# Optimization experiments

Hardware: AMD Instinct MI355X
Metric: run time of the kernel (lower is better)

Reference implementation:

```python
import jax, jax.numpy as jnp
import numpy as np

B, S, D = 4, 2048, 64
H = 16            # num_heads
HD = D // H       # head_dim = 4 (code's misnamed 'num_heads' variable)
EPS = 1e-5        # BatchNorm1d default eps


def setup_inputs() -> dict:
    key = jax.random.key(0)
    ks = jax.random.split(key, 8)
    sc = 1.0 / np.sqrt(D)
    return {
        "x": jax.random.normal(ks[0], (B, S, D), dtype=jnp.float32),
        "Wq": jax.random.normal(ks[1], (D, D), dtype=jnp.float32) * sc,
        "bq": jnp.zeros((D,), dtype=jnp.float32),
        "Wk": jax.random.normal(ks[2], (D, D), dtype=jnp.float32) * sc,
        "bk": jnp.zeros((D,), dtype=jnp.float32),
        "Wv": jax.random.normal(ks[3], (D, D), dtype=jnp.float32) * sc,
        "bv": jnp.zeros((D,), dtype=jnp.float32),
        "gamma": jnp.ones((D,), dtype=jnp.float32),
        "beta": jnp.zeros((D,), dtype=jnp.float32),
    }


def reference(x, Wq, bq, Wk, bk, Wv, bv, gamma, beta):
    # ReLU-activated QKV projections
    Q = jax.nn.relu(jnp.einsum("bsd,de->bse", x, Wq) + bq)
    K = jax.nn.relu(jnp.einsum("bsd,de->bse", x, Wk) + bk)
    V = jax.nn.relu(jnp.einsum("bsd,de->bse", x, Wv) + bv)

    # split(dim=2)->cat(dim=0) is equivalent to head-split reshape [B,S,H,HD]
    Qh = Q.reshape(B, S, H, HD)
    Kh = K.reshape(B, S, H, HD)
    Vh = V.reshape(B, S, H, HD)

    scores = jnp.einsum("bqhd,bkhd->bhqk", Qh, Kh) / jnp.sqrt(jnp.float32(HD))
    attn = jax.nn.softmax(scores, axis=-1)  # dropout_rate = 0.0 -> no-op
    out = jnp.einsum("bhqk,bkhd->bqhd", attn, Vh).reshape(B, S, D)

    # residual
    out = out + x

    # BatchNorm1d(64) in training mode: batch stats over (B, S) per channel
    mean = jnp.mean(out, axis=(0, 1))
    var = jnp.var(out, axis=(0, 1))  # biased variance, as used for normalization
    out = (out - mean) * jax.lax.rsqrt(var + EPS) * gamma + beta
    return out
```

## Files before the change

### kernel.cpp

```cpp
#include <hip/hip_runtime.h>

#define BB 4
#define SS 2048
#define DD 64
#define HH 16
#define HDD 4
#define NBH (BB*HH)
#define NROWS (BB*SS)
#define CHK 512
#define LOG2E_HALF 0.7213475204444817f

typedef float f32x2 __attribute__((ext_vector_type(2)));

__global__ __launch_bounds__(256) void qkv_kernel(
    const float* __restrict__ x,
    const float* __restrict__ Wq, const float* __restrict__ bq,
    const float* __restrict__ Wk, const float* __restrict__ bk,
    const float* __restrict__ Wv, const float* __restrict__ bv,
    float* __restrict__ Q, float* __restrict__ KV)
{
    __shared__ float xs[4 * 64];
    const int tid = threadIdx.x;
    const int row0 = blockIdx.x * 4;

    xs[tid] = x[(size_t)row0 * 64 + tid];
    __syncthreads();

    const int r = tid >> 6;
    const int c = tid & 63;
    const int row = row0 + r;
    const int b = row >> 11;
    const int s = row & (SS - 1);
    const float* xr = &xs[r * 64];

    float aq = bq[c], ak = bk[c], av = bv[c];
    #pragma unroll 16
    for (int k = 0; k < 64; ++k) {
        const float xv = xr[k];
        aq = fmaf(xv, Wq[k * 64 + c], aq);
        ak = fmaf(xv, Wk[k * 64 + c], ak);
        av = fmaf(xv, Wv[k * 64 + c], av);
    }
    aq = fmaxf(aq, 0.0f);
    ak = fmaxf(ak, 0.0f) * LOG2E_HALF;
    av = fmaxf(av, 0.0f);

    const int h = c >> 2, hd = c & 3;
    const size_t bhs = ((size_t)(b * HH + h) * SS + s);
    Q[bhs * 4 + hd] = aq;

    const int p = s >> 1, po = s & 1;
    const size_t pb = ((size_t)(b * HH + h) * (SS / 2) + p) * 16;
    KV[pb + hd * 2 + po] = ak;
    KV[pb + 8 + hd * 2 + po] = av;
}

__global__ __launch_bounds__(256) void attn_bn_kernel(
    const float* __restrict__ Qb, const float* __restrict__ KVb,
    const float* __restrict__ x, float* __restrict__ y,
    float* __restrict__ part2)
{
    __shared__ float4 kvs4[CHK * 4];
    __shared__ float rr[4][8];
    const f32x2* kvs = (const f32x2*)kvs4;

    const int tid = threadIdx.x;
    const int bh = blockIdx.x >> 3;
    const int qt = blockIdx.x & 7;
    const int qrow = qt * 256 + tid;

    const float4 q4 = ((const float4*)Qb)[(size_t)bh * SS + qrow];
    const f32x2 qx = {q4.x, q4.x}, qy = {q4.y, q4.y};
    const f32x2 qz = {q4.z, q4.z}, qw = {q4.w, q4.w};

    f32x2 acx = {0.f, 0.f}, acy = {0.f, 0.f};
    f32x2 acz = {0.f, 0.f}, acw = {0.f, 0.f};
    f32x2 sm = {0.f, 0.f};

    const float4* kvg = (const float4*)(KVb + (size_t)bh * (SS / 2) * 16);

    for (int ch = 0; ch < SS / 2 / CHK; ++ch) {
        __syncthreads();
        #pragma unroll
        for (int i = 0; i < CHK * 4 / 256; ++i)
            kvs4[i * 256 + tid] = kvg[ch * CHK * 4 + i * 256 + tid];
        __syncthreads();

        #pragma unroll 2
        for (int j = 0; j < CHK; ++j) {
            const f32x2 kx = kvs[j * 8 + 0];
            const f32x2 ky = kvs[j * 8 + 1];
            const f32x2 kz = kvs[j * 8 + 2];
            const f32x2 kw = kvs[j * 8 + 3];
            const f32x2 vx = kvs[j * 8 + 4];
            const f32x2 vy = kvs[j * 8 + 5];
            const f32x2 vz = kvs[j * 8 + 6];
            const f32x2 vw = kvs[j * 8 + 7];
            f32x2 s = qx * kx;
            s = __builtin_elementwise_fma(qy, ky, s);
            s = __builtin_elementwise_fma(qz, kz, s);
            s = __builtin_elementwise_fma(qw, kw, s);
            f32x2 e;
            e.x = __builtin_amdgcn_exp2f(s.x);
            e.y = __builtin_amdgcn_exp2f(s.y);
            sm += e;
            acx = __builtin_elementwise_fma(e, vx, acx);
            acy = __builtin_elementwise_fma(e, vy, acy);
            acz = __builtin_elementwise_fma(e, vz, acz);
            acw = __builtin_elementwise_fma(e, vw, acw);
        }
    }

    const float sum = sm.x + sm.y;
    const float inv = 1.0f / sum;
    const int b = bh >> 4, h = bh & 15;
    const size_t o = ((size_t)(b * SS + qrow)) * DD + h * HDD;
    const float4 xr = *(const float4*)(x + o);
    float4 out;
    out.x = fmaf(acx.x + acx.y, inv, xr.x);
    out.y = fmaf(acy.x + acy.y, inv, xr.y);
    out.z = fmaf(acz.x + acz.y, inv, xr.z);
    out.w = fmaf(acw.x + acw.y, inv, xr.w);
    *(float4*)(y + o) = out;

    float v[8] = {out.x, out.y, out.z, out.w,
                  out.x * out.x, out.y * out.y, out.z * out.z, out.w * out.w};
    #pragma unroll
    for (int i = 0; i < 8; ++i) {
        float t = v[i];
        for (int off = 32; off > 0; off >>= 1) t += __shfl_down(t, off);
        v[i] = t;
    }
    const int wid = tid >> 6;
    if ((tid & 63) == 0) {
        #pragma unroll
        for (int i = 0; i < 8; ++i) rr[wid][i] = v[i];
    }
    __syncthreads();
    if (tid < 8) {
        const float t = rr[0][tid] + rr[1][tid] + rr[2][tid] + rr[3][tid];
        const int slot = b * 8 + qt;
        const int i = tid & 3;
        const int c = h * 4 + i;
        if (tid < 4) part2[c * 32 + slot] = t;
        else         part2[2048 + c * 32 + slot] = t;
    }
}

__global__ __launch_bounds__(256) void bn_norm_fused(
    float* __restrict__ y, const float* __restrict__ part2,
    const float* __restrict__ gamma, const float* __restrict__ beta)
{
    __shared__ float st[128];
    const int tid = threadIdx.x;
    if (tid < 128) {
        const int c = tid & 63;
        const float* p = part2 + (tid >> 6) * 2048 + c * 32;
        float s = 0.f;
        #pragma unroll
        for (int i = 0; i < 32; ++i) s += p[i];
        st[tid] = s;
    }
    __syncthreads();

    const int idx = blockIdx.x * 256 + tid;
    const int c0 = (idx & 15) * 4;
    float4 v = ((const float4*)y)[idx];
    const float n = 1.0f / NROWS;
    const float m0 = st[c0] * n,     m1 = st[c0 + 1] * n;
    const float m2 = st[c0 + 2] * n, m3 = st[c0 + 3] * n;
    const float r0 = rsqrtf(st[64 + c0] * n - m0 * m0 + 1e-5f);
    const float r1 = rsqrtf(st[65 + c0] * n - m1 * m1 + 1e-5f);
    const float r2 = rsqrtf(st[66 + c0] * n - m2 * m2 + 1e-5f);
    const float r3 = rsqrtf(st[67 + c0] * n - m3 * m3 + 1e-5f);
    float4 o;
    o.x = fmaf((v.x - m0) * r0, gamma[c0],     beta[c0]);
    o.y = fmaf((v.y - m1) * r1, gamma[c0 + 1], beta[c0 + 1]);
    o.z = fmaf((v.z - m2) * r2, gamma[c0 + 2], beta[c0 + 2]);
    o.w = fmaf((v.w - m3) * r3, gamma[c0 + 3], beta[c0 + 3]);
    ((float4*)y)[idx] = o;
}

extern "C" void kernel_launch(void* const* d_in, const int* in_sizes, int n_in,
                              void* d_out, int out_size, void* d_ws, size_t ws_size,
                              hipStream_t stream)
{
    const float* x     = (const float*)d_in[0];
    const float* Wq    = (const float*)d_in[1];
    const float* bq    = (const float*)d_in[2];
    const float* Wk    = (const float*)d_in[3];
    const float* bk    = (const float*)d_in[4];
    const float* Wv    = (const float*)d_in[5];
    const float* bv    = (const float*)d_in[6];
    const float* gamma = (const float*)d_in[7];
    const float* beta  = (const float*)d_in[8];
    float* out = (float*)d_out;

    float* ws    = (float*)d_ws;
    float* Q     = ws;
    float* KV    = ws + 524288;
    float* part2 = ws + 1572864;

    qkv_kernel<<<NROWS / 4, 256, 0, stream>>>(x, Wq, bq, Wk, bk, Wv, bv, Q, KV);
    attn_bn_kernel<<<NBH * 8, 256, 0, stream>>>(Q, KV, x, out, part2);
    bn_norm_fused<<<NROWS * DD / 1024, 256, 0, stream>>>(out, part2, gamma, beta);
}
```

Before: 119.3 us.

## Split attention over key chunks with atomic-counter last-block reduction

Each attention block now handles two query rows per thread (QR=2), so every K/V value loaded from shared memory is reused across two queries. The key dimension is split into KSPLIT slices across separate blocks. Partial accumulators and sums go to workspace, and the last-arriving block, detected with an atomic counter, combines them and computes the residual and BatchNorm partial sums. The aim is more blocks for better occupancy and more reuse of LDS loads. The cost is extra global traffic for the partials, fence and atomic synchronisation, and a split factor that depends on the workspace size.

```diff
diff --git a/kernel.cpp b/kernel.cpp
--- a/kernel.cpp
+++ b/kernel.cpp
@@ -7,18 +7,25 @@
 #define HDD 4
 #define NBH (BB*HH)
 #define NROWS (BB*SS)
-#define CHK 512
+#define NQ (NBH*SS)
 #define LOG2E_HALF 0.7213475204444817f
 
 typedef float f32x2 __attribute__((ext_vector_type(2)));
+
+#define QR 2
+#define QTN (SS/(256*QR))
+#define NGRP (NBH*QTN)
 
 __global__ __launch_bounds__(256) void qkv_kernel(
     const float* __restrict__ x,
     const float* __restrict__ Wq, const float* __restrict__ bq,
     const float* __restrict__ Wk, const float* __restrict__ bk,
     const float* __restrict__ Wv, const float* __restrict__ bv,
-    float* __restrict__ Q, float* __restrict__ KV)
-{
+    float* __restrict__ Q, float* __restrict__ KV,
+    unsigned int* __restrict__ cnt)
+{
+    if (blockIdx.x == 0) cnt[threadIdx.x] = 0u;
+
     __shared__ float xs[4 * 64];
     const int tid = threadIdx.x;
     const int row0 = blockIdx.x * 4;
@@ -55,95 +62,142 @@
     KV[pb + 8 + hd * 2 + po] = av;
 }
 
-__global__ __launch_bounds__(256) void attn_bn_kernel(
+template<int KSPLIT>
+__global__ __launch_bounds__(256) void attn_kernel(
     const float* __restrict__ Qb, const float* __restrict__ KVb,
     const float* __restrict__ x, float* __restrict__ y,
-    float* __restrict__ part2)
-{
-    __shared__ float4 kvs4[CHK * 4];
+    float* __restrict__ accS, float* __restrict__ sumS,
+    float* __restrict__ part2, unsigned int* __restrict__ cnt)
+{
+    constexpr int PAIRS = SS / 2 / KSPLIT;
+    __shared__ float4 kvs4[PAIRS * 4];
     __shared__ float rr[4][8];
+    __shared__ unsigned int oldv;
     const f32x2* kvs = (const f32x2*)kvs4;
 
     const int tid = threadIdx.x;
-    const int bh = blockIdx.x >> 3;
-    const int qt = blockIdx.x & 7;
-    const int qrow = qt * 256 + tid;
-
-    const float4 q4 = ((const float4*)Qb)[(size_t)bh * SS + qrow];
-    const f32x2 qx = {q4.x, q4.x}, qy = {q4.y, q4.y};
-    const f32x2 qz = {q4.z, q4.z}, qw = {q4.w, q4.w};
-
-    f32x2 acx = {0.f, 0.f}, acy = {0.f, 0.f};
-    f32x2 acz = {0.f, 0.f}, acw = {0.f, 0.f};
-    f32x2 sm = {0.f, 0.f};
-
-    const float4* kvg = (const float4*)(KVb + (size_t)bh * (SS / 2) * 16);
-
-    for (int ch = 0; ch < SS / 2 / CHK; ++ch) {
-        __syncthreads();
-        #pragma unroll
-        for (int i = 0; i < CHK * 4 / 256; ++i)
-            kvs4[i * 256 + tid] = kvg[ch * CHK * 4 + i * 256 + tid];
-        __syncthreads();
-
-        #pragma unroll 2
-        for (int j = 0; j < CHK; ++j) {
-            const f32x2 kx = kvs[j * 8 + 0];
-            const f32x2 ky = kvs[j * 8 + 1];
-            const f32x2 kz = kvs[j * 8 + 2];
-            const f32x2 kw = kvs[j * 8 + 3];
-            const f32x2 vx = kvs[j * 8 + 4];
-            const f32x2 vy = kvs[j * 8 + 5];
-            const f32x2 vz = kvs[j * 8 + 6];
-            const f32x2 vw = kvs[j * 8 + 7];
-            f32x2 s = qx * kx;
-            s = __builtin_elementwise_fma(qy, ky, s);
-            s = __builtin_elementwise_fma(qz, kz, s);
-            s = __builtin_elementwise_fma(qw, kw, s);
+    int blk = blockIdx.x;
+    const int ks = blk / (NBH * QTN);
+    blk -= ks * (NBH * QTN);
+    const int bh = blk / QTN;
+    const int qt = blk - bh * QTN;
+
+    const float4* kvg = (const float4*)(KVb + ((size_t)bh * (SS / 2) + (size_t)ks * PAIRS) * 16);
+    #pragma unroll
+    for (int i = 0; i < PAIRS * 4 / 256; ++i)
+        kvs4[i * 256 + tid] = kvg[i * 256 + tid];
+
+    f32x2 qx[QR], qy[QR], qz[QR], qw[QR];
+    #pragma unroll
+    for (int r = 0; r < QR; ++r) {
+        const int qrow = qt * (256 * QR) + r * 256 + tid;
+        const float4 q = ((const float4*)Qb)[(size_t)bh * SS + qrow];
+        qx[r] = {q.x, q.x}; qy[r] = {q.y, q.y};
+        qz[r] = {q.z, q.z}; qw[r] = {q.w, q.w};
+    }
+
+    f32x2 acx[QR], acy[QR], acz[QR], acw[QR], sm[QR];
+    #pragma unroll
+    for (int r = 0; r < QR; ++r) {
+        acx[r] = {0.f, 0.f}; acy[r] = {0.f, 0.f};
+        acz[r] = {0.f, 0.f}; acw[r] = {0.f, 0.f};
+        sm[r] = {0.f, 0.f};
+    }
+
+    __syncthreads();
+
+    #pragma unroll 2
+    for (int j = 0; j < PAIRS; ++j) {
+        const f32x2 kx = kvs[j * 8 + 0];
+        const f32x2 ky = kvs[j * 8 + 1];
+        const f32x2 kz = kvs[j * 8 + 2];
+        const f32x2 kw = kvs[j * 8 + 3];
+        const f32x2 vx = kvs[j * 8 + 4];
+        const f32x2 vy = kvs[j * 8 + 5];
+        const f32x2 vz = kvs[j * 8 + 6];
+        const f32x2 vw = kvs[j * 8 + 7];
+        #pragma unroll
+        for (int r = 0; r < QR; ++r) {
+            f32x2 s = qx[r] * kx;
+            s = __builtin_elementwise_fma(qy[r], ky, s);
+            s = __builtin_elementwise_fma(qz[r], kz, s);
+            s = __builtin_elementwise_fma(qw[r], kw, s);
             f32x2 e;
             e.x = __builtin_amdgcn_exp2f(s.x);
             e.y = __builtin_amdgcn_exp2f(s.y);
-            sm += e;
-            acx = __builtin_elementwise_fma(e, vx, acx);
-            acy = __builtin_elementwise_fma(e, vy, acy);
-            acz = __builtin_elementwise_fma(e, vz, acz);
-            acw = __builtin_elementwise_fma(e, vw, acw);
+            sm[r] += e;
+            acx[r] = __builtin_elementwise_fma(e, vx, acx[r]);
+            acy[r] = __builtin_elementwise_fma(e, vy, acy[r]);
+            acz[r] = __builtin_elementwise_fma(e, vz, acz[r]);
+            acw[r] = __builtin_elementwise_fma(e, vw, acw[r]);
         }
     }
 
-    const float sum = sm.x + sm.y;
-    const float inv = 1.0f / sum;
+    #pragma unroll
+    for (int r = 0; r < QR; ++r) {
+        const int qrow = qt * (256 * QR) + r * 256 + tid;
+        const size_t qi = (size_t)ks * NQ + (size_t)bh * SS + qrow;
+        float4 acc = {acx[r].x + acx[r].y, acy[r].x + acy[r].y,
+                      acz[r].x + acz[r].y, acw[r].x + acw[r].y};
+        ((float4*)accS)[qi] = acc;
+        sumS[qi] = sm[r].x + sm[r].y;
+    }
+
+    __threadfence();
+    __syncthreads();
+    if (tid == 0)
+        oldv = __hip_atomic_fetch_add(&cnt[bh * QTN + qt], 1u,
+                                      __ATOMIC_ACQ_REL, __HIP_MEMORY_SCOPE_AGENT);
+    __syncthreads();
+    if (oldv != (unsigned)(KSPLIT - 1)) return;
+
+    __threadfence();
     const int b = bh >> 4, h = bh & 15;
-    const size_t o = ((size_t)(b * SS + qrow)) * DD + h * HDD;
-    const float4 xr = *(const float4*)(x + o);
-    float4 out;
-    out.x = fmaf(acx.x + acx.y, inv, xr.x);
-    out.y = fmaf(acy.x + acy.y, inv, xr.y);
-    out.z = fmaf(acz.x + acz.y, inv, xr.z);
-    out.w = fmaf(acw.x + acw.y, inv, xr.w);
-    *(float4*)(y + o) = out;
-
-    float v[8] = {out.x, out.y, out.z, out.w,
-                  out.x * out.x, out.y * out.y, out.z * out.z, out.w * out.w};
+    float vv[8] = {0.f, 0.f, 0.f, 0.f, 0.f, 0.f, 0.f, 0.f};
+    #pragma unroll
+    for (int r = 0; r < QR; ++r) {
+        const int qrow = qt * (256 * QR) + r * 256 + tid;
+        const size_t qbase = (size_t)bh * SS + qrow;
+        float4 a = ((const float4*)accS)[qbase];
+        float s = sumS[qbase];
+        #pragma unroll
+        for (int k = 1; k < KSPLIT; ++k) {
+            const float4 a2 = ((const float4*)accS)[(size_t)k * NQ + qbase];
+            a.x += a2.x; a.y += a2.y; a.z += a2.z; a.w += a2.w;
+            s += sumS[(size_t)k * NQ + qbase];
+        }
+        const float inv = 1.0f / s;
+        const size_t o = ((size_t)(b * SS + qrow)) * DD + h * HDD;
+        const float4 xr = *(const float4*)(x + o);
+        float4 out;
+        out.x = fmaf(a.x, inv, xr.x);
+        out.y = fmaf(a.y, inv, xr.y);
+        out.z = fmaf(a.z, inv, xr.z);
+        out.w = fmaf(a.w, inv, xr.w);
+        *(float4*)(y + o) = out;
+        vv[0] += out.x; vv[1] += out.y; vv[2] += out.z; vv[3] += out.w;
+        vv[4] += out.x * out.x; vv[5] += out.y * out.y;
+        vv[6] += out.z * out.z; vv[7] += out.w * out.w;
+    }
     #pragma unroll
     for (int i = 0; i < 8; ++i) {
-        float t = v[i];
+        float t = vv[i];
         for (int off = 32; off > 0; off >>= 1) t += __shfl_down(t, off);
-        v[i] = t;
+        vv[i] = t;
     }
     const int wid = tid >> 6;
     if ((tid & 63) == 0) {
         #pragma unroll
-        for (int i = 0; i < 8; ++i) rr[wid][i] = v[i];
+        for (int i = 0; i < 8; ++i) rr[wid][i] = vv[i];
     }
     __syncthreads();
     if (tid < 8) {
         const float t = rr[0][tid] + rr[1][tid] + rr[2][tid] + rr[3][tid];
-        const int slot = b * 8 + qt;
+        const int slot = b * QTN + qt;
         const int i = tid & 3;
         const int c = h * 4 + i;
-        if (tid < 4) part2[c * 32 + slot] = t;
-        else         part2[2048 + c * 32 + slot] = t;
+        if (tid < 4) part2[c * 16 + slot] = t;
+        else         part2[2048 + c * 16 + slot] = t;
     }
 }
 
@@ -155,10 +209,10 @@
     const int tid = threadIdx.x;
     if (tid < 128) {
         const int c = tid & 63;
-        const float* p = part2 + (tid >> 6) * 2048 + c * 32;
+        const float* p = part2 + (tid >> 6) * 2048 + c * 16;
         float s = 0.f;
         #pragma unroll
-        for (int i = 0; i < 32; ++i) s += p[i];
+        for (int i = 0; i < 16; ++i) s += p[i];
         st[tid] = s;
     }
     __syncthreads();
@@ -196,12 +250,35 @@
     const float* beta  = (const float*)d_in[8];
     float* out = (float*)d_out;
 
-    float* ws    = (float*)d_ws;
-    float* Q     = ws;
-    float* KV    = ws + 524288;
-    float* part2 = ws + 1572864;
-
-    qkv_kernel<<<NROWS / 4, 256, 0, stream>>>(x, Wq, bq, Wk, bk, Wv, bv, Q, KV);
-    attn_bn_kernel<<<NBH * 8, 256, 0, stream>>>(Q, KV, x, out, part2);
+    float* ws = (float*)d_ws;
+    float* Q  = ws;
+    float* KV = ws + 524288;
+
+    const size_t base = 524288 + 1048576;
+    auto need = [](int kk) {
+        return (size_t)(524288 + 1048576 + (size_t)kk * NQ * 5 + 4096 + 512) * 4;
+    };
+
+    int KS = 1;
+    if (ws_size >= need(8))      KS = 8;
+    else if (ws_size >= need(4)) KS = 4;
+    else if (ws_size >= need(2)) KS = 2;
+
+    float* accS  = ws + base;
+    float* sumS  = accS + (size_t)KS * NQ * 4;
+    float* part2 = sumS + (size_t)KS * NQ;
+    unsigned int* cnt = (unsigned int*)(part2 + 4096);
+
+    qkv_kernel<<<NROWS / 4, 256, 0, stream>>>(x, Wq, bq, Wk, bk, Wv, bv, Q, KV, cnt);
+
+    if (KS == 8)
+        attn_kernel<8><<<8 * NGRP, 256, 0, stream>>>(Q, KV, x, out, accS, sumS, part2, cnt);
+    else if (KS == 4)
+        attn_kernel<4><<<4 * NGRP, 256, 0, stream>>>(Q, KV, x, out, accS, sumS, part2, cnt);
+    else if (KS == 2)
+        attn_kernel<2><<<2 * NGRP, 256, 0, stream>>>(Q, KV, x, out, accS, sumS, part2, cnt);
+    else
+        attn_kernel<1><<<1 * NGRP, 256, 0, stream>>>(Q, KV, x, out, accS, sumS, part2, cnt);
+
     bn_norm_fused<<<NROWS * DD / 1024, 256, 0, stream>>>(out, part2, gamma, beta);
 }
```

Measured after the change: 302.6 us. +153.7%, slower.

## Split key range across four waves per query row and reduce in LDS

Applied to the files above, without the earlier changes.

Each attention block now handles 64 query rows, and its four waves each process a quarter of every key/value chunk. Partial sums are combined through shared memory before the residual add and statistics write. This raises the grid from 512 to 2048 blocks so more of the GPU's compute units are kept busy. The cost is four times more global loads of K/V per query, an extra LDS reduction, more partial-sum slots for the BatchNorm stage, and three idle waves during the epilogue.

```diff
diff --git a/kernel.cpp b/kernel.cpp
--- a/kernel.cpp
+++ b/kernel.cpp
@@ -7,10 +7,14 @@
 #define HDD 4
 #define NBH (BB*HH)
 #define NROWS (BB*SS)
-#define CHK 512
 #define LOG2E_HALF 0.7213475204444817f
 
 typedef float f32x2 __attribute__((ext_vector_type(2)));
+
+#define CHKP 256
+#define PPT  (CHKP/4)
+#define NCHK (SS/2/CHKP)
+#define SLOTS 128
 
 __global__ __launch_bounds__(256) void qkv_kernel(
     const float* __restrict__ x,
@@ -55,19 +59,21 @@
     KV[pb + 8 + hd * 2 + po] = av;
 }
 
-__global__ __launch_bounds__(256) void attn_bn_kernel(
+__global__ __launch_bounds__(256) void attn_fused(
     const float* __restrict__ Qb, const float* __restrict__ KVb,
     const float* __restrict__ x, float* __restrict__ y,
     float* __restrict__ part2)
 {
-    __shared__ float4 kvs4[CHK * 4];
-    __shared__ float rr[4][8];
+    __shared__ float4 kvs4[CHKP * 4];
+    __shared__ float red[4][64][5];
     const f32x2* kvs = (const f32x2*)kvs4;
 
     const int tid = threadIdx.x;
-    const int bh = blockIdx.x >> 3;
-    const int qt = blockIdx.x & 7;
-    const int qrow = qt * 256 + tid;
+    const int bh = blockIdx.x >> 5;
+    const int rt = blockIdx.x & 31;
+    const int r  = tid & 63;
+    const int p  = tid >> 6;
+    const int qrow = rt * 64 + r;
 
     const float4 q4 = ((const float4*)Qb)[(size_t)bh * SS + qrow];
     const f32x2 qx = {q4.x, q4.x}, qy = {q4.y, q4.y};
@@ -79,23 +85,24 @@
 
     const float4* kvg = (const float4*)(KVb + (size_t)bh * (SS / 2) * 16);
 
-    for (int ch = 0; ch < SS / 2 / CHK; ++ch) {
+    for (int ch = 0; ch < NCHK; ++ch) {
         __syncthreads();
         #pragma unroll
-        for (int i = 0; i < CHK * 4 / 256; ++i)
-            kvs4[i * 256 + tid] = kvg[ch * CHK * 4 + i * 256 + tid];
+        for (int i = 0; i < CHKP * 4 / 256; ++i)
+            kvs4[i * 256 + tid] = kvg[ch * CHKP * 4 + i * 256 + tid];
         __syncthreads();
 
+        const f32x2* kp = kvs + (size_t)p * PPT * 8;
         #pragma unroll 2
-        for (int j = 0; j < CHK; ++j) {
-            const f32x2 kx = kvs[j * 8 + 0];
-            const f32x2 ky = kvs[j * 8 + 1];
-            const f32x2 kz = kvs[j * 8 + 2];
-            const f32x2 kw = kvs[j * 8 + 3];
-            const f32x2 vx = kvs[j * 8 + 4];
-            const f32x2 vy = kvs[j * 8 + 5];
-            const f32x2 vz = kvs[j * 8 + 6];
-            const f32x2 vw = kvs[j * 8 + 7];
+        for (int j = 0; j < PPT; ++j) {
+            const f32x2 kx = kp[j * 8 + 0];
+            const f32x2 ky = kp[j * 8 + 1];
+            const f32x2 kz = kp[j * 8 + 2];
+            const f32x2 kw = kp[j * 8 + 3];
+            const f32x2 vx = kp[j * 8 + 4];
+            const f32x2 vy = kp[j * 8 + 5];
+            const f32x2 vz = kp[j * 8 + 6];
+            const f32x2 vw = kp[j * 8 + 7];
             f32x2 s = qx * kx;
             s = __builtin_elementwise_fma(qy, ky, s);
             s = __builtin_elementwise_fma(qz, kz, s);
@@ -111,39 +118,49 @@
         }
     }
 
-    const float sum = sm.x + sm.y;
-    const float inv = 1.0f / sum;
+    red[p][r][0] = acx.x + acx.y;
+    red[p][r][1] = acy.x + acy.y;
+    red[p][r][2] = acz.x + acz.y;
+    red[p][r][3] = acw.x + acw.y;
+    red[p][r][4] = sm.x + sm.y;
+    __syncthreads();
+    if (tid >= 64) return;
+
+    float4 a;
+    a.x = red[0][r][0] + red[1][r][0] + red[2][r][0] + red[3][r][0];
+    a.y = red[0][r][1] + red[1][r][1] + red[2][r][1] + red[3][r][1];
+    a.z = red[0][r][2] + red[1][r][2] + red[2][r][2] + red[3][r][2];
+    a.w = red[0][r][3] + red[1][r][3] + red[2][r][3] + red[3][r][3];
+    const float s = red[0][r][4] + red[1][r][4] + red[2][r][4] + red[3][r][4];
+    const float inv = 1.0f / s;
+
     const int b = bh >> 4, h = bh & 15;
     const size_t o = ((size_t)(b * SS + qrow)) * DD + h * HDD;
     const float4 xr = *(const float4*)(x + o);
     float4 out;
-    out.x = fmaf(acx.x + acx.y, inv, xr.x);
-    out.y = fmaf(acy.x + acy.y, inv, xr.y);
-    out.z = fmaf(acz.x + acz.y, inv, xr.z);
-    out.w = fmaf(acw.x + acw.y, inv, xr.w);
+    out.x = fmaf(a.x, inv, xr.x);
+    out.y = fmaf(a.y, inv, xr.y);
+    out.z = fmaf(a.z, inv, xr.z);
+    out.w = fmaf(a.w, inv, xr.w);
     *(float4*)(y + o) = out;
 
-    float v[8] = {out.x, out.y, out.z, out.w,
-                  out.x * out.x, out.y * out.y, out.z * out.z, out.w * out.w};
+    float vv[8] = {out.x, out.y, out.z, out.w,
+                   out.x * out.x, out.y * out.y, out.z * out.z, out.w * out.w};
     #pragma unroll
     for (int i = 0; i < 8; ++i) {
-        float t = v[i];
+        float t = vv[i];
+        #pragma unroll
         for (int off = 32; off > 0; off >>= 1) t += __shfl_down(t, off);
-        v[i] = t;
-    }
-    const int wid = tid >> 6;
-    if ((tid & 63) == 0) {
+        vv[i] = t;
+    }
+    if (r == 0) {
+        const int slot = b * 32 + rt;
+        const int c0 = h * 4;
         #pragma unroll
-        for (int i = 0; i < 8; ++i) rr[wid][i] = v[i];
-    }
-    __syncthreads();
-    if (tid < 8) {
-        const float t = rr[0][tid] + rr[1][tid] + rr[2][tid] + rr[3][tid];
-        const int slot = b * 8 + qt;
-        const int i = tid & 3;
-        const int c = h * 4 + i;
-        if (tid < 4) part2[c * 32 + slot] = t;
-        else         part2[2048 + c * 32 + slot] = t;
+        for (int i = 0; i < 4; ++i) {
+            part2[(c0 + i) * SLOTS + slot] = vv[i];
+            part2[64 * SLOTS + (c0 + i) * SLOTS + slot] = vv[4 + i];
+        }
     }
 }
 
@@ -155,10 +172,10 @@
     const int tid = threadIdx.x;
     if (tid < 128) {
         const int c = tid & 63;
-        const float* p = part2 + (tid >> 6) * 2048 + c * 32;
+        const float* p = part2 + (tid >> 6) * (64 * SLOTS) + c * SLOTS;
         float s = 0.f;
-        #pragma unroll
-        for (int i = 0; i < 32; ++i) s += p[i];
+        #pragma unroll 8
+        for (int i = 0; i < SLOTS; ++i) s += p[i];
         st[tid] = s;
     }
     __syncthreads();
@@ -202,6 +219,6 @@
     float* part2 = ws + 1572864;
 
     qkv_kernel<<<NROWS / 4, 256, 0, stream>>>(x, Wq, bq, Wk, bk, Wv, bv, Q, KV);
-    attn_bn_kernel<<<NBH * 8, 256, 0, stream>>>(Q, KV, x, out, part2);
+    attn_fused<<<NBH * 32, 256, 0, stream>>>(Q, KV, x, out, part2);
     bn_norm_fused<<<NROWS * DD / 1024, 256, 0, stream>>>(out, part2, gamma, beta);
 }
```

Measured after the change: 118.1 us. No clear change (-1.0%).
